# Kernel optimization log

Hardware: AMD Instinct MI355X
Metric: run time of the kernel (lower is better)

The kernel has to match this reference:

```python
import math
import jax, jax.numpy as jnp
import numpy as np

CH_IN = 32
CH_OUT = 32
K = 3
P = 4
STRIDE = 2
ITER = 3
FINAL_LAMBDA = 0.01
EPS = 1e-8
LOG_2PI = math.log(2.0 * math.pi)


def _conv_stat(x):
    # Conv2d(ch_in, ch_in, K, stride, bias=False) with constant weight 1/K^2, VALID padding
    w = jnp.full((CH_IN, CH_IN, K, K), 1.0 / (K * K), dtype=x.dtype)
    return jax.lax.conv_general_dilated(
        x, w, window_strides=(STRIDE, STRIDE), padding='VALID',
        dimension_numbers=('NCHW', 'OIHW', 'NCHW'))


def setup_inputs() -> dict:
    key = jax.random.key(0)
    k1, k2, k3 = jax.random.split(key, 3)
    bs, h_in, w_in = 64, 14, 14
    ho = (h_in - K) // STRIDE + 1  # 6
    x = jax.random.normal(k1, (bs, CH_IN, h_in, w_in, P, P), dtype=jnp.float32)
    a = jax.random.uniform(k2, (bs, CH_IN, h_in, w_in), dtype=jnp.float32)
    w = jax.random.uniform(k3, (1, CH_IN, ho, ho, P, P, CH_OUT), dtype=jnp.float32)
    b_u = jnp.zeros((CH_OUT,), jnp.float32)
    b_a = jnp.zeros((CH_OUT,), jnp.float32)
    return {"x": x, "a": a, "w": w, "b_u": b_u, "b_a": b_a}


def _voting(x, w):
    # x: (bs, ci, h_in, w_in, P, P) -> v: (bs, ci, h_out, w_out, P, P, co)
    bs, ci, h, wd = x.shape[:4]
    # raw reshape, matching torch .view on contiguous tensor
    xc = _conv_stat(x.reshape(bs * P * P, ci, h, wd))
    ho, wo = xc.shape[2], xc.shape[3]
    xc = xc.reshape(bs, ci, ho, wo, P, P)
    # repeat x along ch_out, then raw reshape (P,P,co)->(co,P,P), same as torch .view
    xv = jnp.broadcast_to(xc[..., None], (bs, ci, ho, wo, P, P, CH_OUT))
    xv = xv.reshape(bs, ci, ho, wo, CH_OUT, P, P)
    wv = jnp.broadcast_to(w, (bs, ci, ho, wo, P, P, CH_OUT))
    wv = wv.reshape(bs, ci, ho, wo, CH_OUT, P, P)
    v = jnp.matmul(xv, wv)  # batched 4x4 matmuls
    return v.reshape(bs, ci, ho, wo, P, P, CH_OUT)


def _m_step(a, r, v, lambd, b_u, b_a):
    # a: (N, ci, 1)  r: (N, ci, co)  v: (N, ci, co, pp)
    r = (r * a)[..., None] + EPS                                  # (N, ci, co, 1)
    r_sum = jnp.sum(r, axis=1, keepdims=True)                     # (N, 1, co, 1)
    mu = jnp.sum(r * v, axis=1, keepdims=True) / r_sum            # (N, 1, co, pp)
    sig_sq = jnp.sum(r * (v - mu) ** 2, axis=1, keepdims=True) / r_sum + EPS
    cost = (b_u.reshape(1, 1, CH_OUT, 1) + 0.5 * jnp.log(sig_sq)) * r_sum
    a_out = jax.nn.sigmoid(lambd * (b_a.reshape(1, 1, CH_OUT, 1)
                                    - jnp.sum(cost, axis=3, keepdims=True)))
    return a_out, mu, sig_sq


def _e_step(mu, sig_sq, a_out, v):
    p_ln = -(v - mu) ** 2 / (2.0 * sig_sq) - 0.5 * jnp.log(sig_sq) - 0.5 * LOG_2PI
    ap_ln = jnp.sum(p_ln, axis=3, keepdims=True) + jnp.log(a_out)  # (N, ci, co, 1)
    return jax.nn.softmax(ap_ln[..., 0], axis=2)                   # (N, ci, co)


def _em_routing(v, a, b_u, b_a):
    bs, ci, h, wd, p1, p2, co = v.shape
    # raw reshapes, matching torch .view
    vv = v.reshape(bs * h * wd, ci, co, p1 * p2)
    av = a.reshape(bs * h * wd, ci)[..., None]
    r = jnp.full((bs * h * wd, ci, co), 1.0 / co, dtype=v.dtype)
    for it in range(ITER):
        lambd = FINAL_LAMBDA * (1.0 - 0.95 ** (1 + it))
        a_out, mu, sig_sq = _m_step(av, r, vv, lambd, b_u, b_a)
        if it < ITER - 1:
            r = _e_step(mu, sig_sq, a_out, vv)
    mu = mu.reshape(bs, co, h, wd, p1, p2)
    a_out = a_out.reshape(bs, co, h, wd)
    return mu, a_out


def reference(x, a, w, b_u, b_a):
    v = _voting(x, w)
    a_conv = _conv_stat(a)
    mu, a_out = _em_routing(v, a_conv, b_u, b_a)
    return mu, a_out
```

## Files before the change

kernel.cpp:

```cpp
#include <hip/hip_runtime.h>
#include <math.h>


#define EPSF 1e-8f

typedef float f2 __attribute__((ext_vector_type(2)));
typedef unsigned u32x2 __attribute__((ext_vector_type(2)));

__device__ __forceinline__ float rcpf(float x) { return __builtin_amdgcn_rcpf(x); }

__device__ __forceinline__ float reduce4(float x) {
#if __has_builtin(__builtin_amdgcn_permlane16_swap) && __has_builtin(__builtin_amdgcn_permlane32_swap)
    unsigned xu = __float_as_uint(x);
    u32x2 p = __builtin_amdgcn_permlane16_swap(xu, xu, false, false);
    float s = __uint_as_float(p.x) + __uint_as_float(p.y);
    unsigned su = __float_as_uint(s);
    u32x2 q = __builtin_amdgcn_permlane32_swap(su, su, false, false);
    return __uint_as_float(q.x) + __uint_as_float(q.y);
#else
    x += __shfl_xor(x, 16);
    x += __shfl_xor(x, 32);
    return x;
#endif
}

__device__ __forceinline__ float dpp_xor1(float x) {
    return __int_as_float(__builtin_amdgcn_update_dpp(
        0, __float_as_int(x), 0xB1, 0xF, 0xF, true));
}
__device__ __forceinline__ float dpp_xor2(float x) {
    return __int_as_float(__builtin_amdgcn_update_dpp(
        0, __float_as_int(x), 0x4E, 0xF, 0xF, true));
}

__global__ __launch_bounds__(256) void pre_kernel(
        const float* __restrict__ x, const float* __restrict__ a,
        const float* __restrict__ w,
        float* __restrict__ S, float* __restrict__ A, float* __restrict__ Wsum) {
    int bid = blockIdx.x;
    if (bid < 1088) {
        __shared__ float plane[6272];
        __shared__ float bsum[196];
        const int t = threadIdx.x;
        const float* src = (bid < 1024) ? (x + (size_t)bid * 6272)
                                        : (a + (size_t)(bid - 1024) * 6272);
        for (int k = t; k < 1568; k += 256)
            *(float4*)&plane[k * 4] = *(const float4*)(src + k * 4);
        __syncthreads();
        if (t < 196) {
            float s = 0.f;
#pragma unroll
            for (int c = 0; c < 32; ++c) s += plane[c * 196 + t];
            bsum[t] = s;
        }
        __syncthreads();
        if (t < 36) {
            int oy = t / 6, ox = t - oy * 6;
            const float* q = &bsum[oy * 28 + ox * 2];
            float s = (q[0] + q[1] + q[2]) + (q[14] + q[15] + q[16])
                    + (q[28] + q[29] + q[30]);
            s *= (1.0f / 9.0f);
            if (bid < 1024) S[bid * 36 + t] = s;
            else            A[(bid - 1024) * 36 + t] = s;
        }
    } else {
        int wi = (bid - 1088) * 256 + threadIdx.x;
        int sp = wi >> 12;
        int rr = wi & 4095;
        int ci = rr >> 7, co = (rr >> 2) & 31, j = rr & 3;
        int B = sp * 32 + ci;
        int cc = B / 36;
        int rem = B - cc * 36;
        int wbase = cc * 18432 + (rem / 6) * 3072 + (rem % 6) * 512 + co * 16 + j;
        Wsum[wi] = w[wbase] + w[wbase + 4] + w[wbase + 8] + w[wbase + 12];
    }
}

__global__ __launch_bounds__(128, 4) void em_kernel(
        const float* __restrict__ bu, const float* __restrict__ ba,
        const float* __restrict__ S, const float* __restrict__ A,
        const float* __restrict__ Wsum, float* __restrict__ out) {
    __shared__ float lgb[33 * 32];

    const int t = threadIdx.x;
    const int w = t >> 6;
    const int lane = t & 63;
    const int o = w * 16 + (lane & 15);
    const int cq = lane >> 4;
    const int c0 = cq * 8;
    const int n = blockIdx.x;
    const int bq = n / 36;
    const int sp = n - bq * 36;

    const int hc = o >> 1;
    f2 V2[8][2];
    float avr[8], r[8];
    const float* Wn = Wsum + sp * 4096;
#pragma unroll
    for (int cl = 0; cl < 8; ++cl) {
        int c = c0 + cl;
        int B = sp * 32 + c;
        int cc = B / 36;
        int rem = B - cc * 36;
        int off = cc * 576 + (rem / 6) * 96 + (rem % 6) * 16 + hc;
        int hi = off / 1152;
        int lo = off - hi * 1152;
        float sv = S[(bq * 16 + hi) * 36 + lo % 36];
        float4 w4 = *(const float4*)(Wn + c * 128 + o * 4);
        V2[cl][0] = (f2){sv * w4.x, sv * w4.y};
        V2[cl][1] = (f2){sv * w4.z, sv * w4.w};
        avr[cl] = A[bq * 36 + (32 * sp + c) % 36];
        r[cl] = 0.03125f;
    }
    const float bu16 = 16.0f * bu[o];
    const float ba_o = ba[o];
    f2 mu2[2], q2[2];
    float aout = 0.f;
    const float lambdas[3] = {5.0e-4f, 9.75e-4f, 1.42625e-3f};

    for (int it = 0; it < 3; ++it) {
        float rp[8];
#pragma unroll
        for (int cl = 0; cl < 8; ++cl) rp[cl] = r[cl] * avr[cl] + EPSF;
        float rs = ((rp[0] + rp[1]) + (rp[2] + rp[3]))
                 + ((rp[4] + rp[5]) + (rp[6] + rp[7]));
        rs = reduce4(rs);
        float rinv = rcpf(rs);
#pragma unroll
        for (int p = 0; p < 2; ++p) {
            f2 a0 = {0.f, 0.f}, a1 = {0.f, 0.f};
#pragma unroll
            for (int cl = 0; cl < 8; cl += 2) {
                a0 += rp[cl] * V2[cl][p];
                a1 += rp[cl + 1] * V2[cl + 1][p];
            }
            f2 m = a0 + a1;
            m.x = reduce4(m.x);
            m.y = reduce4(m.y);
            mu2[p] = m * rinv;
        }
        float L;
        {
            f2 sgv[2];
#pragma unroll
            for (int p = 0; p < 2; ++p) {
                f2 a0 = {0.f, 0.f}, a1 = {0.f, 0.f};
#pragma unroll
                for (int cl = 0; cl < 8; cl += 2) {
                    f2 d0 = V2[cl][p] - mu2[p];
                    f2 d1 = V2[cl + 1][p] - mu2[p];
                    a0 += (d0 * d0) * rp[cl];
                    a1 += (d1 * d1) * rp[cl + 1];
                }
                f2 sg = a0 + a1;
                sg.x = reduce4(sg.x);
                sg.y = reduce4(sg.y);
                sgv[p] = sg * rinv + EPSF;
                q2[p] = (f2){2.0f * rcpf(sgv[p].x), 2.0f * rcpf(sgv[p].y)};
            }
            L = __logf((sgv[0].x * sgv[0].y) * (sgv[1].x * sgv[1].y));
        }
        float cost = (bu16 + 2.0f * L) * rs;
        float z = lambdas[it] * (ba_o - cost);

        if (it < 2) {
            float la = -__logf(1.0f + __expf(-z));
            float T = la - 2.0f * L;
#pragma unroll
            for (int cl = 0; cl < 8; ++cl) {
                f2 d0 = V2[cl][0] - mu2[0];
                f2 d1 = V2[cl][1] - mu2[1];
                f2 s2 = (d0 * d0) * q2[0] + (d1 * d1) * q2[1];
                lgb[(c0 + cl) * 33 + o] = T - (s2.x + s2.y);
            }
            __syncthreads();
            {
                int cT = t >> 2, q = t & 3;
                float* rowp = &lgb[cT * 33 + q * 8];
                float4 u0 = *(float4*)(rowp);
                float4 u1 = *(float4*)(rowp + 4);
                float m0 = fmaxf(fmaxf(u0.x, u0.y), fmaxf(u0.z, u0.w));
                float m1 = fmaxf(fmaxf(u1.x, u1.y), fmaxf(u1.z, u1.w));
                float m = fmaxf(m0, m1);
                m = fmaxf(m, dpp_xor1(m));
                m = fmaxf(m, dpp_xor2(m));
                u0.x = __expf(u0.x - m); u0.y = __expf(u0.y - m);
                u0.z = __expf(u0.z - m); u0.w = __expf(u0.w - m);
                u1.x = __expf(u1.x - m); u1.y = __expf(u1.y - m);
                u1.z = __expf(u1.z - m); u1.w = __expf(u1.w - m);
                float s0 = (u0.x + u0.y) + (u0.z + u0.w);
                float s1 = (u1.x + u1.y) + (u1.z + u1.w);
                float ssum = s0 + s1;
                ssum += dpp_xor1(ssum);
                ssum += dpp_xor2(ssum);
                float inv = rcpf(ssum);
                u0.x *= inv; u0.y *= inv; u0.z *= inv; u0.w *= inv;
                u1.x *= inv; u1.y *= inv; u1.z *= inv; u1.w *= inv;
                *(float4*)(rowp)     = u0;
                *(float4*)(rowp + 4) = u1;
            }
            __syncthreads();
#pragma unroll
            for (int cl = 0; cl < 8; ++cl)
                r[cl] = lgb[(c0 + cl) * 33 + o];
        } else {
            aout = rcpf(1.0f + __expf(-z));
        }
    }

    float4 val = {mu2[0].x, mu2[0].y, mu2[1].x, mu2[1].y};
    float4* po = (float4*)(out + n * 512 + o * 16);
    po[cq] = val;
    if (cq == 0) out[1179648 + n * 32 + o] = aout;
}

extern "C" void kernel_launch(void* const* d_in, const int* in_sizes, int n_in,
                              void* d_out, int out_size, void* d_ws, size_t ws_size,
                              hipStream_t stream) {
    const float* x = (const float*)d_in[0];
    const float* a = (const float*)d_in[1];
    const float* w = (const float*)d_in[2];
    const float* bu = (const float*)d_in[3];
    const float* ba = (const float*)d_in[4];
    float* out = (float*)d_out;

    float* S    = (float*)d_ws;
    float* A    = S + 36864;
    float* Wsum = A + 2304;

    pre_kernel<<<1088 + 576, 256, 0, stream>>>(x, a, w, S, A, Wsum);
    em_kernel<<<2304, 128, 0, stream>>>(bu, ba, S, A, Wsum, out);
}
```

Before: 22.14 us.

## Split EM routing across 256 threads with four input capsules per thread

Each EM block now runs 256 threads instead of 128. Every thread handles 4 input channels for one output channel instead of 8. Cross-thread sums gain an extra row-rotate DPP step (reduce8), and the softmax reduces over 8 lanes using a half-row mirror DPP. The aim is more waves per block, which shortens the serial per-thread work and hides latency. In exchange there are extra shuffle steps, a larger block to synchronise, and tighter occupancy limits from the new launch bounds.

```diff
diff --git a/kernel.cpp b/kernel.cpp
--- a/kernel.cpp
+++ b/kernel.cpp
@@ -9,7 +9,25 @@
 
 __device__ __forceinline__ float rcpf(float x) { return __builtin_amdgcn_rcpf(x); }
 
-__device__ __forceinline__ float reduce4(float x) {
+__device__ __forceinline__ float dpp_ror8(float x) {
+    return __int_as_float(__builtin_amdgcn_update_dpp(
+        0, __float_as_int(x), 0x128, 0xF, 0xF, true));
+}
+__device__ __forceinline__ float dpp_xor1(float x) {
+    return __int_as_float(__builtin_amdgcn_update_dpp(
+        0, __float_as_int(x), 0xB1, 0xF, 0xF, true));
+}
+__device__ __forceinline__ float dpp_xor2(float x) {
+    return __int_as_float(__builtin_amdgcn_update_dpp(
+        0, __float_as_int(x), 0x4E, 0xF, 0xF, true));
+}
+__device__ __forceinline__ float dpp_mirror7(float x) {
+    return __int_as_float(__builtin_amdgcn_update_dpp(
+        0, __float_as_int(x), 0x141, 0xF, 0xF, true));
+}
+
+__device__ __forceinline__ float reduce8(float x) {
+    x += dpp_ror8(x);
 #if __has_builtin(__builtin_amdgcn_permlane16_swap) && __has_builtin(__builtin_amdgcn_permlane32_swap)
     unsigned xu = __float_as_uint(x);
     u32x2 p = __builtin_amdgcn_permlane16_swap(xu, xu, false, false);
@@ -22,15 +40,6 @@
     x += __shfl_xor(x, 32);
     return x;
 #endif
-}
-
-__device__ __forceinline__ float dpp_xor1(float x) {
-    return __int_as_float(__builtin_amdgcn_update_dpp(
-        0, __float_as_int(x), 0xB1, 0xF, 0xF, true));
-}
-__device__ __forceinline__ float dpp_xor2(float x) {
-    return __int_as_float(__builtin_amdgcn_update_dpp(
-        0, __float_as_int(x), 0x4E, 0xF, 0xF, true));
 }
 
 __global__ __launch_bounds__(256) void pre_kernel(
@@ -76,28 +85,28 @@
     }
 }
 
-__global__ __launch_bounds__(128, 4) void em_kernel(
+__global__ __launch_bounds__(256, 6) void em_kernel(
         const float* __restrict__ bu, const float* __restrict__ ba,
         const float* __restrict__ S, const float* __restrict__ A,
         const float* __restrict__ Wsum, float* __restrict__ out) {
     __shared__ float lgb[33 * 32];
 
     const int t = threadIdx.x;
-    const int w = t >> 6;
+    const int wv = t >> 6;
     const int lane = t & 63;
-    const int o = w * 16 + (lane & 15);
-    const int cq = lane >> 4;
-    const int c0 = cq * 8;
+    const int o = wv * 8 + (lane & 7);
+    const int s = lane >> 3;
+    const int c0 = s * 4;
     const int n = blockIdx.x;
     const int bq = n / 36;
     const int sp = n - bq * 36;
 
     const int hc = o >> 1;
-    f2 V2[8][2];
-    float avr[8], r[8];
+    f2 V2[4][2];
+    float avr[4], r[4];
     const float* Wn = Wsum + sp * 4096;
 #pragma unroll
-    for (int cl = 0; cl < 8; ++cl) {
+    for (int cl = 0; cl < 4; ++cl) {
         int c = c0 + cl;
         int B = sp * 32 + c;
         int cc = B / 36;
@@ -119,24 +128,19 @@
     const float lambdas[3] = {5.0e-4f, 9.75e-4f, 1.42625e-3f};
 
     for (int it = 0; it < 3; ++it) {
-        float rp[8];
-#pragma unroll
-        for (int cl = 0; cl < 8; ++cl) rp[cl] = r[cl] * avr[cl] + EPSF;
-        float rs = ((rp[0] + rp[1]) + (rp[2] + rp[3]))
-                 + ((rp[4] + rp[5]) + (rp[6] + rp[7]));
-        rs = reduce4(rs);
+        float rp[4];
+#pragma unroll
+        for (int cl = 0; cl < 4; ++cl) rp[cl] = r[cl] * avr[cl] + EPSF;
+        float rs = (rp[0] + rp[1]) + (rp[2] + rp[3]);
+        rs = reduce8(rs);
         float rinv = rcpf(rs);
 #pragma unroll
         for (int p = 0; p < 2; ++p) {
-            f2 a0 = {0.f, 0.f}, a1 = {0.f, 0.f};
-#pragma unroll
-            for (int cl = 0; cl < 8; cl += 2) {
-                a0 += rp[cl] * V2[cl][p];
-                a1 += rp[cl + 1] * V2[cl + 1][p];
-            }
+            f2 a0 = rp[0] * V2[0][p] + rp[1] * V2[1][p];
+            f2 a1 = rp[2] * V2[2][p] + rp[3] * V2[3][p];
             f2 m = a0 + a1;
-            m.x = reduce4(m.x);
-            m.y = reduce4(m.y);
+            m.x = reduce8(m.x);
+            m.y = reduce8(m.y);
             mu2[p] = m * rinv;
         }
         float L;
@@ -144,17 +148,14 @@
             f2 sgv[2];
 #pragma unroll
             for (int p = 0; p < 2; ++p) {
-                f2 a0 = {0.f, 0.f}, a1 = {0.f, 0.f};
-#pragma unroll
-                for (int cl = 0; cl < 8; cl += 2) {
-                    f2 d0 = V2[cl][p] - mu2[p];
-                    f2 d1 = V2[cl + 1][p] - mu2[p];
-                    a0 += (d0 * d0) * rp[cl];
-                    a1 += (d1 * d1) * rp[cl + 1];
-                }
-                f2 sg = a0 + a1;
-                sg.x = reduce4(sg.x);
-                sg.y = reduce4(sg.y);
+                f2 d0 = V2[0][p] - mu2[p];
+                f2 d1 = V2[1][p] - mu2[p];
+                f2 d2 = V2[2][p] - mu2[p];
+                f2 d3 = V2[3][p] - mu2[p];
+                f2 sg = ((d0 * d0) * rp[0] + (d1 * d1) * rp[1])
+                      + ((d2 * d2) * rp[2] + (d3 * d3) * rp[3]);
+                sg.x = reduce8(sg.x);
+                sg.y = reduce8(sg.y);
                 sgv[p] = sg * rinv + EPSF;
                 q2[p] = (f2){2.0f * rcpf(sgv[p].x), 2.0f * rcpf(sgv[p].y)};
             }
@@ -167,7 +168,7 @@
             float la = -__logf(1.0f + __expf(-z));
             float T = la - 2.0f * L;
 #pragma unroll
-            for (int cl = 0; cl < 8; ++cl) {
+            for (int cl = 0; cl < 4; ++cl) {
                 f2 d0 = V2[cl][0] - mu2[0];
                 f2 d1 = V2[cl][1] - mu2[1];
                 f2 s2 = (d0 * d0) * q2[0] + (d1 * d1) * q2[1];
@@ -175,33 +176,26 @@
             }
             __syncthreads();
             {
-                int cT = t >> 2, q = t & 3;
-                float* rowp = &lgb[cT * 33 + q * 8];
-                float4 u0 = *(float4*)(rowp);
-                float4 u1 = *(float4*)(rowp + 4);
-                float m0 = fmaxf(fmaxf(u0.x, u0.y), fmaxf(u0.z, u0.w));
-                float m1 = fmaxf(fmaxf(u1.x, u1.y), fmaxf(u1.z, u1.w));
-                float m = fmaxf(m0, m1);
+                int cT = t >> 3, q = t & 7;
+                float* rowp = &lgb[cT * 33 + q * 4];
+                float4 u = *(float4*)(rowp);
+                float m = fmaxf(fmaxf(u.x, u.y), fmaxf(u.z, u.w));
                 m = fmaxf(m, dpp_xor1(m));
                 m = fmaxf(m, dpp_xor2(m));
-                u0.x = __expf(u0.x - m); u0.y = __expf(u0.y - m);
-                u0.z = __expf(u0.z - m); u0.w = __expf(u0.w - m);
-                u1.x = __expf(u1.x - m); u1.y = __expf(u1.y - m);
-                u1.z = __expf(u1.z - m); u1.w = __expf(u1.w - m);
-                float s0 = (u0.x + u0.y) + (u0.z + u0.w);
-                float s1 = (u1.x + u1.y) + (u1.z + u1.w);
-                float ssum = s0 + s1;
+                m = fmaxf(m, dpp_mirror7(m));
+                u.x = __expf(u.x - m); u.y = __expf(u.y - m);
+                u.z = __expf(u.z - m); u.w = __expf(u.w - m);
+                float ssum = (u.x + u.y) + (u.z + u.w);
                 ssum += dpp_xor1(ssum);
                 ssum += dpp_xor2(ssum);
+                ssum += dpp_mirror7(ssum);
                 float inv = rcpf(ssum);
-                u0.x *= inv; u0.y *= inv; u0.z *= inv; u0.w *= inv;
-                u1.x *= inv; u1.y *= inv; u1.z *= inv; u1.w *= inv;
-                *(float4*)(rowp)     = u0;
-                *(float4*)(rowp + 4) = u1;
+                u.x *= inv; u.y *= inv; u.z *= inv; u.w *= inv;
+                *(float4*)(rowp) = u;
             }
             __syncthreads();
 #pragma unroll
-            for (int cl = 0; cl < 8; ++cl)
+            for (int cl = 0; cl < 4; ++cl)
                 r[cl] = lgb[(c0 + cl) * 33 + o];
         } else {
             aout = rcpf(1.0f + __expf(-z));
@@ -210,8 +204,8 @@
 
     float4 val = {mu2[0].x, mu2[0].y, mu2[1].x, mu2[1].y};
     float4* po = (float4*)(out + n * 512 + o * 16);
-    po[cq] = val;
-    if (cq == 0) out[1179648 + n * 32 + o] = aout;
+    if (s < 4) po[s] = val;
+    if (s == 0) out[1179648 + n * 32 + o] = aout;
 }
 
 extern "C" void kernel_launch(void* const* d_in, const int* in_sizes, int n_in,
@@ -229,5 +223,5 @@
     float* Wsum = A + 2304;
 
     pre_kernel<<<1088 + 576, 256, 0, stream>>>(x, a, w, S, A, Wsum);
-    em_kernel<<<2304, 128, 0, stream>>>(bu, ba, S, A, Wsum, out);
-}
+    em_kernel<<<2304, 256, 0, stream>>>(bu, ba, S, A, Wsum, out);
+}
```

Result: slower. 23.38 us (+5.6%).

## Map one EM position per wavefront and do softmax with DPP/permlane instead of LDS

Applied to the files above, without the earlier changes.

Restructures em_kernel so each 64-lane wavefront handles a whole spatial position, with 32 output capsules times 2 halves of the 32 input capsules and 16 inputs per lane. Four positions are packed per 256-thread block. The cross-input softmax now runs in registers through DPP row reductions and permlane16 swaps, removing the shared-memory buffer and both __syncthreads per iteration. Partial sums over inputs are combined with a single permlane32 swap. In exchange, per-thread register use doubles, which may lower occupancy, and each lane now does 16 serial exp and reduction chains.

```diff
diff --git a/kernel.cpp b/kernel.cpp
--- a/kernel.cpp
+++ b/kernel.cpp
@@ -9,28 +9,40 @@
 
 __device__ __forceinline__ float rcpf(float x) { return __builtin_amdgcn_rcpf(x); }
 
-__device__ __forceinline__ float reduce4(float x) {
-#if __has_builtin(__builtin_amdgcn_permlane16_swap) && __has_builtin(__builtin_amdgcn_permlane32_swap)
-    unsigned xu = __float_as_uint(x);
-    u32x2 p = __builtin_amdgcn_permlane16_swap(xu, xu, false, false);
-    float s = __uint_as_float(p.x) + __uint_as_float(p.y);
-    unsigned su = __float_as_uint(s);
-    u32x2 q = __builtin_amdgcn_permlane32_swap(su, su, false, false);
-    return __uint_as_float(q.x) + __uint_as_float(q.y);
-#else
-    x += __shfl_xor(x, 16);
-    x += __shfl_xor(x, 32);
+template <int CTRL>
+__device__ __forceinline__ float dpp_mov(float x) {
+    return __int_as_float(__builtin_amdgcn_update_dpp(
+        0, __float_as_int(x), CTRL, 0xF, 0xF, true));
+}
+
+__device__ __forceinline__ float row_sum16(float x) {
+    x += dpp_mov<0x121>(x);
+    x += dpp_mov<0x122>(x);
+    x += dpp_mov<0x124>(x);
+    x += dpp_mov<0x128>(x);
     return x;
-#endif
-}
-
-__device__ __forceinline__ float dpp_xor1(float x) {
-    return __int_as_float(__builtin_amdgcn_update_dpp(
-        0, __float_as_int(x), 0xB1, 0xF, 0xF, true));
-}
-__device__ __forceinline__ float dpp_xor2(float x) {
-    return __int_as_float(__builtin_amdgcn_update_dpp(
-        0, __float_as_int(x), 0x4E, 0xF, 0xF, true));
+}
+__device__ __forceinline__ float row_max16(float x) {
+    x = fmaxf(x, dpp_mov<0x121>(x));
+    x = fmaxf(x, dpp_mov<0x122>(x));
+    x = fmaxf(x, dpp_mov<0x124>(x));
+    x = fmaxf(x, dpp_mov<0x128>(x));
+    return x;
+}
+__device__ __forceinline__ float pl16_sum(float x) {
+    unsigned u = __float_as_uint(x);
+    u32x2 p = __builtin_amdgcn_permlane16_swap(u, u, false, false);
+    return __uint_as_float(p.x) + __uint_as_float(p.y);
+}
+__device__ __forceinline__ float pl16_max(float x) {
+    unsigned u = __float_as_uint(x);
+    u32x2 p = __builtin_amdgcn_permlane16_swap(u, u, false, false);
+    return fmaxf(__uint_as_float(p.x), __uint_as_float(p.y));
+}
+__device__ __forceinline__ float pl32_sum(float x) {
+    unsigned u = __float_as_uint(x);
+    u32x2 p = __builtin_amdgcn_permlane32_swap(u, u, false, false);
+    return __uint_as_float(p.x) + __uint_as_float(p.y);
 }
 
 __global__ __launch_bounds__(256) void pre_kernel(
@@ -76,29 +88,26 @@
     }
 }
 
-__global__ __launch_bounds__(128, 4) void em_kernel(
+__global__ __launch_bounds__(256, 3) void em_kernel(
         const float* __restrict__ bu, const float* __restrict__ ba,
         const float* __restrict__ S, const float* __restrict__ A,
         const float* __restrict__ Wsum, float* __restrict__ out) {
-    __shared__ float lgb[33 * 32];
-
     const int t = threadIdx.x;
-    const int w = t >> 6;
+    const int g = t >> 6;
     const int lane = t & 63;
-    const int o = w * 16 + (lane & 15);
-    const int cq = lane >> 4;
-    const int c0 = cq * 8;
-    const int n = blockIdx.x;
+    const int h = lane >> 5;
+    const int o = lane & 31;
+    const int n = blockIdx.x * 4 + g;
     const int bq = n / 36;
     const int sp = n - bq * 36;
 
     const int hc = o >> 1;
-    f2 V2[8][2];
-    float avr[8], r[8];
+    f2 V2[16][2];
+    float avr[16], r[16];
     const float* Wn = Wsum + sp * 4096;
 #pragma unroll
-    for (int cl = 0; cl < 8; ++cl) {
-        int c = c0 + cl;
+    for (int cl = 0; cl < 16; ++cl) {
+        int c = h * 16 + cl;
         int B = sp * 32 + c;
         int cc = B / 36;
         int rem = B - cc * 36;
@@ -119,24 +128,31 @@
     const float lambdas[3] = {5.0e-4f, 9.75e-4f, 1.42625e-3f};
 
     for (int it = 0; it < 3; ++it) {
-        float rp[8];
-#pragma unroll
-        for (int cl = 0; cl < 8; ++cl) rp[cl] = r[cl] * avr[cl] + EPSF;
-        float rs = ((rp[0] + rp[1]) + (rp[2] + rp[3]))
-                 + ((rp[4] + rp[5]) + (rp[6] + rp[7]));
-        rs = reduce4(rs);
+        float rp[16];
+#pragma unroll
+        for (int cl = 0; cl < 16; ++cl) rp[cl] = r[cl] * avr[cl] + EPSF;
+        float rs;
+        {
+            float t0 = (rp[0] + rp[1]) + (rp[2] + rp[3]);
+            float t1 = (rp[4] + rp[5]) + (rp[6] + rp[7]);
+            float t2 = (rp[8] + rp[9]) + (rp[10] + rp[11]);
+            float t3 = (rp[12] + rp[13]) + (rp[14] + rp[15]);
+            rs = pl32_sum((t0 + t1) + (t2 + t3));
+        }
         float rinv = rcpf(rs);
 #pragma unroll
         for (int p = 0; p < 2; ++p) {
-            f2 a0 = {0.f, 0.f}, a1 = {0.f, 0.f};
-#pragma unroll
-            for (int cl = 0; cl < 8; cl += 2) {
+            f2 a0 = {0.f, 0.f}, a1 = {0.f, 0.f}, a2 = {0.f, 0.f}, a3 = {0.f, 0.f};
+#pragma unroll
+            for (int cl = 0; cl < 16; cl += 4) {
                 a0 += rp[cl] * V2[cl][p];
                 a1 += rp[cl + 1] * V2[cl + 1][p];
-            }
-            f2 m = a0 + a1;
-            m.x = reduce4(m.x);
-            m.y = reduce4(m.y);
+                a2 += rp[cl + 2] * V2[cl + 2][p];
+                a3 += rp[cl + 3] * V2[cl + 3][p];
+            }
+            f2 m = (a0 + a1) + (a2 + a3);
+            m.x = pl32_sum(m.x);
+            m.y = pl32_sum(m.y);
             mu2[p] = m * rinv;
         }
         float L;
@@ -144,17 +160,21 @@
             f2 sgv[2];
 #pragma unroll
             for (int p = 0; p < 2; ++p) {
-                f2 a0 = {0.f, 0.f}, a1 = {0.f, 0.f};
-#pragma unroll
-                for (int cl = 0; cl < 8; cl += 2) {
+                f2 a0 = {0.f, 0.f}, a1 = {0.f, 0.f}, a2 = {0.f, 0.f}, a3 = {0.f, 0.f};
+#pragma unroll
+                for (int cl = 0; cl < 16; cl += 4) {
                     f2 d0 = V2[cl][p] - mu2[p];
                     f2 d1 = V2[cl + 1][p] - mu2[p];
+                    f2 d2 = V2[cl + 2][p] - mu2[p];
+                    f2 d3 = V2[cl + 3][p] - mu2[p];
                     a0 += (d0 * d0) * rp[cl];
                     a1 += (d1 * d1) * rp[cl + 1];
+                    a2 += (d2 * d2) * rp[cl + 2];
+                    a3 += (d3 * d3) * rp[cl + 3];
                 }
-                f2 sg = a0 + a1;
-                sg.x = reduce4(sg.x);
-                sg.y = reduce4(sg.y);
+                f2 sg = (a0 + a1) + (a2 + a3);
+                sg.x = pl32_sum(sg.x);
+                sg.y = pl32_sum(sg.y);
                 sgv[p] = sg * rinv + EPSF;
                 q2[p] = (f2){2.0f * rcpf(sgv[p].x), 2.0f * rcpf(sgv[p].y)};
             }
@@ -166,43 +186,21 @@
         if (it < 2) {
             float la = -__logf(1.0f + __expf(-z));
             float T = la - 2.0f * L;
-#pragma unroll
-            for (int cl = 0; cl < 8; ++cl) {
+            float lg[16];
+#pragma unroll
+            for (int cl = 0; cl < 16; ++cl) {
                 f2 d0 = V2[cl][0] - mu2[0];
                 f2 d1 = V2[cl][1] - mu2[1];
                 f2 s2 = (d0 * d0) * q2[0] + (d1 * d1) * q2[1];
-                lgb[(c0 + cl) * 33 + o] = T - (s2.x + s2.y);
-            }
-            __syncthreads();
-            {
-                int cT = t >> 2, q = t & 3;
-                float* rowp = &lgb[cT * 33 + q * 8];
-                float4 u0 = *(float4*)(rowp);
-                float4 u1 = *(float4*)(rowp + 4);
-                float m0 = fmaxf(fmaxf(u0.x, u0.y), fmaxf(u0.z, u0.w));
-                float m1 = fmaxf(fmaxf(u1.x, u1.y), fmaxf(u1.z, u1.w));
-                float m = fmaxf(m0, m1);
-                m = fmaxf(m, dpp_xor1(m));
-                m = fmaxf(m, dpp_xor2(m));
-                u0.x = __expf(u0.x - m); u0.y = __expf(u0.y - m);
-                u0.z = __expf(u0.z - m); u0.w = __expf(u0.w - m);
-                u1.x = __expf(u1.x - m); u1.y = __expf(u1.y - m);
-                u1.z = __expf(u1.z - m); u1.w = __expf(u1.w - m);
-                float s0 = (u0.x + u0.y) + (u0.z + u0.w);
-                float s1 = (u1.x + u1.y) + (u1.z + u1.w);
-                float ssum = s0 + s1;
-                ssum += dpp_xor1(ssum);
-                ssum += dpp_xor2(ssum);
-                float inv = rcpf(ssum);
-                u0.x *= inv; u0.y *= inv; u0.z *= inv; u0.w *= inv;
-                u1.x *= inv; u1.y *= inv; u1.z *= inv; u1.w *= inv;
-                *(float4*)(rowp)     = u0;
-                *(float4*)(rowp + 4) = u1;
-            }
-            __syncthreads();
-#pragma unroll
-            for (int cl = 0; cl < 8; ++cl)
-                r[cl] = lgb[(c0 + cl) * 33 + o];
+                lg[cl] = T - (s2.x + s2.y);
+            }
+#pragma unroll
+            for (int cl = 0; cl < 16; ++cl) {
+                float m = pl16_max(row_max16(lg[cl]));
+                float e = __expf(lg[cl] - m);
+                float ssum = pl16_sum(row_sum16(e));
+                r[cl] = e * rcpf(ssum);
+            }
         } else {
             aout = rcpf(1.0f + __expf(-z));
         }
@@ -210,8 +208,9 @@
 
     float4 val = {mu2[0].x, mu2[0].y, mu2[1].x, mu2[1].y};
     float4* po = (float4*)(out + n * 512 + o * 16);
-    po[cq] = val;
-    if (cq == 0) out[1179648 + n * 32 + o] = aout;
+    po[2 * h] = val;
+    po[2 * h + 1] = val;
+    if (h == 0) out[1179648 + n * 32 + o] = aout;
 }
 
 extern "C" void kernel_launch(void* const* d_in, const int* in_sizes, int n_in,
@@ -229,5 +228,5 @@
     float* Wsum = A + 2304;
 
     pre_kernel<<<1088 + 576, 256, 0, stream>>>(x, a, w, S, A, Wsum);
-    em_kernel<<<2304, 128, 0, stream>>>(bu, ba, S, A, Wsum, out);
-}
+    em_kernel<<<576, 256, 0, stream>>>(bu, ba, S, A, Wsum, out);
+}
```

Result: slower. 36.10 us (+63.1%).
